# Kernel tuning notes

Hardware: AMD Instinct MI355X
Metric: run time of the kernel (lower is better)

## Reference

```python
import jax, jax.numpy as jnp
import numpy as np

N = 100000          # nodes
E = 1600000         # edges (avg degree 16)
F_IN = 128          # input node features
H1, C1 = 8, 8       # conv1: 8 heads, 8 channels/head -> 64 concat
NUM_CLASSES = 40    # conv2: 1 head, 40 channels
EPS = 1e-16         # PyG softmax denominator epsilon
NEG_SLOPE = 0.2     # PyG GATConv default leaky_relu slope


def setup_inputs() -> dict:
    key = jax.random.key(0)
    ks = jax.random.split(key, 12)
    x = jax.random.normal(ks[0], (N, F_IN), jnp.float32)
    edge_index = jax.random.randint(ks[1], (2, E), 0, N, dtype=jnp.int64)
    edge_attr = jax.random.normal(ks[2], (E, 1), jnp.float32)
    # layer 1 params (Glorot-ish scaling)
    s1 = 1.0 / np.sqrt(F_IN)
    W1 = jax.random.normal(ks[3], (F_IN, H1 * C1), jnp.float32) * s1
    a_src1 = jax.random.normal(ks[4], (H1, C1), jnp.float32) * (1.0 / np.sqrt(C1))
    a_dst1 = jax.random.normal(ks[5], (H1, C1), jnp.float32) * (1.0 / np.sqrt(C1))
    b1 = jnp.zeros((H1 * C1,), jnp.float32)
    # layer 2 params: in = 64 (conv1 concat output), 1 head, NUM_CLASSES channels
    s2 = 1.0 / np.sqrt(H1 * C1)
    W2 = jax.random.normal(ks[6], (H1 * C1, NUM_CLASSES), jnp.float32) * s2
    a_src2 = jax.random.normal(ks[7], (1, NUM_CLASSES), jnp.float32) * (1.0 / np.sqrt(NUM_CLASSES))
    a_dst2 = jax.random.normal(ks[8], (1, NUM_CLASSES), jnp.float32) * (1.0 / np.sqrt(NUM_CLASSES))
    b2 = jnp.zeros((NUM_CLASSES,), jnp.float32)
    return {"x": x, "edge_index": edge_index, "edge_attr": edge_attr,
            "W1": W1, "a_src1": a_src1, "a_dst1": a_dst1, "b1": b1,
            "W2": W2, "a_src2": a_src2, "a_dst2": a_dst2, "b2": b2}


def gat_conv(x, src, dst, W, a_s, a_d, b, heads, out_ch):
    """PyG GATConv: linear -> per-edge leaky-relu attention -> dst softmax -> scatter-add."""
    n = x.shape[0]
    h = (x @ W).reshape(n, heads, out_ch)                 # [N,H,C]
    alpha_s = jnp.sum(h * a_s, axis=-1)                   # [N,H]
    alpha_d = jnp.sum(h * a_d, axis=-1)                   # [N,H]
    e = jax.nn.leaky_relu(alpha_s[src] + alpha_d[dst], NEG_SLOPE)  # [Etot,H]
    # segment softmax over incoming edges per destination node
    m = jax.ops.segment_max(e, dst, num_segments=n)       # [N,H]
    e = jnp.exp(e - m[dst])
    denom = jax.ops.segment_sum(e, dst, num_segments=n)   # [N,H]
    alpha = e / (denom[dst] + EPS)                        # [Etot,H]
    msg = h[src] * alpha[:, :, None]                      # [Etot,H,C]
    out = jax.ops.segment_sum(msg, dst, num_segments=n)   # [N,H,C]
    return out.reshape(n, heads * out_ch) + b             # concat heads + bias


def reference(x, edge_index, edge_attr, W1, a_src1, a_dst1, b1, W2, a_src2, a_dst2, b2):
    n = x.shape[0]
    # PyG GATConv adds self-loops by default
    loops = jnp.arange(n, dtype=edge_index.dtype)
    src = jnp.concatenate([edge_index[0], loops])
    dst = jnp.concatenate([edge_index[1], loops])
    x = x.astype(jnp.float32)
    x1 = jax.nn.elu(gat_conv(x, src, dst, W1, a_src1, a_dst1, b1, H1, C1))
    x2 = jax.nn.elu(gat_conv(x1, src, dst, W2, a_src2, a_dst2, b2, 1, NUM_CLASSES))
    return x2
```

## Files before the change

### kernel.cpp

```cpp
#include <hip/hip_runtime.h>
#include <math.h>

#define NN 100000
#define NE 1600000
#define NETOT (NE + NN)
#define FIN 128
#define H1N 8
#define D1 64
#define NC 40
#define LNT 64
#define LOG2E 1.44269504088896f

#define BSH 9
#define BNODES 512
#define NBUC ((NN + BNODES - 1) / BNODES)
#define EPB 4096
#define NBLKA ((NE + EPB - 1) / EPB)
#define BCAP 9216

__device__ __forceinline__ float leakyf(float x) { return x >= 0.0f ? x : 0.2f * x; }
__device__ __forceinline__ float eluf(float x)   { return x > 0.0f ? x : expm1f(x); }
__device__ __forceinline__ float exp2fast(float x) { return __builtin_amdgcn_exp2f(x); }

__device__ __forceinline__ unsigned short f2bf(float f) {
  unsigned u = __float_as_uint(f);
  u += 0x7fffu + ((u >> 16) & 1u);
  return (unsigned short)(u >> 16);
}
__device__ __forceinline__ float bflo(unsigned u) { return __uint_as_float(u << 16); }
__device__ __forceinline__ float bfhi(unsigned u) { return __uint_as_float(u & 0xffff0000u); }

__global__ void k_detect(const long long* __restrict__ ei, int* __restrict__ flag) {
  if (blockIdx.x == 0 && threadIdx.x == 0) {
    int is64 = 1;
    for (int i = 0; i < 16; ++i) {
      long long v = ei[i];
      if (v < 0 || v >= NN) is64 = 0;
    }
    *flag = is64;
  }
}

__global__ __launch_bounds__(256) void k_passA(const void* __restrict__ ei,
                        const int* __restrict__ flag,
                        unsigned int* __restrict__ subbuf, int* __restrict__ bcnt) {
  __shared__ unsigned int   pay[EPB];
  __shared__ unsigned short bk[EPB];
  __shared__ unsigned int   spay[EPB];
  __shared__ unsigned short sbk[EPB];
  __shared__ int hist[256];
  __shared__ int lstart[256];
  __shared__ int cur[256];
  __shared__ int gbase[256];
  int t = threadIdx.x;
  int e0 = blockIdx.x * EPB;
  int cnt = min(EPB, NE - e0);
  hist[t] = 0;
  __syncthreads();
  bool f64 = (*flag) != 0;
  for (int i = t; i < cnt; i += 256) {
    int s, d;
    if (f64) {
      const long long* p = (const long long*)ei;
      s = (int)p[e0 + i]; d = (int)p[NE + e0 + i];
    } else {
      const int* p = (const int*)ei;
      s = p[e0 + i]; d = p[NE + e0 + i];
    }
    int b = d >> BSH;
    pay[i] = ((unsigned)s << BSH) | (unsigned)(d & (BNODES - 1));
    bk[i] = (unsigned short)b;
    atomicAdd(&hist[b], 1);
  }
  __syncthreads();
  int v = hist[t];
  lstart[t] = v;
  __syncthreads();
  for (int st = 1; st < 256; st <<= 1) {
    int xv = (t >= st) ? lstart[t - st] : 0;
    __syncthreads();
    lstart[t] += xv;
    __syncthreads();
  }
  int excl = lstart[t] - v;
  __syncthreads();
  lstart[t] = excl;
  cur[t] = excl;
  gbase[t] = (v > 0) ? atomicAdd(&bcnt[t], v) : 0;
  __syncthreads();
  for (int i = t; i < cnt; i += 256) {
    int b = bk[i];
    int pos = atomicAdd(&cur[b], 1);
    spay[pos] = pay[i];
    sbk[pos] = (unsigned short)b;
  }
  __syncthreads();
  for (int i = t; i < cnt; i += 256) {
    int b = sbk[i];
    int o = gbase[b] + (i - lstart[b]);
    if (o < BCAP) subbuf[(size_t)b * BCAP + o] = spay[i];
  }
}

__global__ void k_bucketsum(const int* __restrict__ bcnt, int* __restrict__ bucket_base,
                            int* __restrict__ row_start) {
  __shared__ int sh[256];
  int t = threadIdx.x;
  int tot = 0;
  if (t < NBUC) {
    int d0 = t << BSH;
    int nloc = min(BNODES, NN - d0);
    tot = nloc + min(bcnt[t], BCAP);
  }
  sh[t] = tot;
  __syncthreads();
  for (int s = 1; s < 256; s <<= 1) {
    int x = (t >= s) ? sh[t - s] : 0;
    __syncthreads();
    sh[t] += x;
    __syncthreads();
  }
  if (t < NBUC) bucket_base[t] = sh[t] - tot;
  if (t == NBUC - 1) row_start[NN] = sh[t];
}

__global__ __launch_bounds__(256) void k_passB(const int* __restrict__ bcnt,
                       const unsigned int* __restrict__ subbuf,
                       const int* __restrict__ bucket_base,
                       int* __restrict__ row_start, int* __restrict__ csr) {
  __shared__ int hist[BNODES];
  __shared__ int ps[256];
  __shared__ int cur[BNODES];
  int b = blockIdx.x, t = threadIdx.x;
  int d0 = b << BSH;
  int nloc = min(BNODES, NN - d0);
  hist[t] = 0; hist[t + 256] = 0;
  __syncthreads();
  int cnt = min(bcnt[b], BCAP);
  const unsigned int* sb = subbuf + (size_t)b * BCAP;
  for (int i = t; i < cnt; i += 256)
    atomicAdd(&hist[sb[i] & (BNODES - 1)], 1);
  __syncthreads();
  int j0 = 2 * t, j1 = 2 * t + 1;
  int s0 = (j0 < nloc) ? hist[j0] + 1 : 0;
  int s1 = (j1 < nloc) ? hist[j1] + 1 : 0;
  int pairsum = s0 + s1;
  ps[t] = pairsum;
  __syncthreads();
  for (int s = 1; s < 256; s <<= 1) {
    int x = (t >= s) ? ps[t - s] : 0;
    __syncthreads();
    ps[t] += x;
    __syncthreads();
  }
  int excl = ps[t] - pairsum + bucket_base[b];
  if (j0 < nloc) {
    row_start[d0 + j0] = excl;
    csr[excl] = d0 + j0;
    cur[j0] = excl + 1;
  }
  if (j1 < nloc) {
    int rs = excl + s0;
    row_start[d0 + j1] = rs;
    csr[rs] = d0 + j1;
    cur[j1] = rs + 1;
  }
  __syncthreads();
  for (int i = t; i < cnt; i += 256) {
    unsigned u = sb[i];
    int pos = atomicAdd(&cur[u & (BNODES - 1)], 1);
    csr[pos] = (int)(u >> BSH);
  }
}

#define XS1(node, k) xs[(node) * FIN + ((k) ^ ((node) & 31))]
__global__ void k_lin1(const float* __restrict__ x, const float* __restrict__ W,
                       const float* __restrict__ aw_s, const float* __restrict__ aw_d,
                       unsigned short* __restrict__ h, float* __restrict__ als,
                       float* __restrict__ ald) {
  __shared__ float ws[FIN * D1];
  __shared__ float xs[LNT * FIN];
  int t = threadIdx.x;
  int base = blockIdx.x * LNT;
  for (int i = t; i < FIN * D1; i += 256) ws[i] = W[i];
  for (int i = t; i < LNT * FIN; i += 256) {
    int node = i >> 7, k = i & 127;
    int gn = base + node;
    if (gn >= NN) gn = NN - 1;
    XS1(node, k) = x[(size_t)gn * FIN + k];
  }
  __syncthreads();
  int head = t & 7, ng = t >> 3;
  int n0l = ng * 2, n1l = n0l + 1;
  float acc0[8] = {0, 0, 0, 0, 0, 0, 0, 0};
  float acc1[8] = {0, 0, 0, 0, 0, 0, 0, 0};
  #pragma unroll 4
  for (int k = 0; k < FIN; ++k) {
    float x0 = XS1(n0l, k);
    float x1v = XS1(n1l, k);
    const float4* wr = (const float4*)&ws[k * D1 + head * 8];
    float4 wa = wr[0], wb = wr[1];
    acc0[0] = fmaf(x0, wa.x, acc0[0]); acc1[0] = fmaf(x1v, wa.x, acc1[0]);
    acc0[1] = fmaf(x0, wa.y, acc0[1]); acc1[1] = fmaf(x1v, wa.y, acc1[1]);
    acc0[2] = fmaf(x0, wa.z, acc0[2]); acc1[2] = fmaf(x1v, wa.z, acc1[2]);
    acc0[3] = fmaf(x0, wa.w, acc0[3]); acc1[3] = fmaf(x1v, wa.w, acc1[3]);
    acc0[4] = fmaf(x0, wb.x, acc0[4]); acc1[4] = fmaf(x1v, wb.x, acc1[4]);
    acc0[5] = fmaf(x0, wb.y, acc0[5]); acc1[5] = fmaf(x1v, wb.y, acc1[5]);
    acc0[6] = fmaf(x0, wb.z, acc0[6]); acc1[6] = fmaf(x1v, wb.z, acc1[6]);
    acc0[7] = fmaf(x0, wb.w, acc0[7]); acc1[7] = fmaf(x1v, wb.w, acc1[7]);
  }
  int n0 = base + n0l, n1 = base + n1l;
  float aws[8], awd[8];
  #pragma unroll
  for (int c = 0; c < 8; ++c) { aws[c] = aw_s[head * 8 + c]; awd[c] = aw_d[head * 8 + c]; }
  if (n0 < NN) {
    float s = 0.f, d = 0.f;
    #pragma unroll
    for (int c = 0; c < 8; ++c) {
      h[(size_t)n0 * D1 + head * 8 + c] = f2bf(acc0[c]);
      s = fmaf(acc0[c], aws[c], s);
      d = fmaf(acc0[c], awd[c], d);
    }
    als[n0 * H1N + head] = s * LOG2E;
    ald[n0 * H1N + head] = d * LOG2E;
  }
  if (n1 < NN) {
    float s = 0.f, d = 0.f;
    #pragma unroll
    for (int c = 0; c < 8; ++c) {
      h[(size_t)n1 * D1 + head * 8 + c] = f2bf(acc1[c]);
      s = fmaf(acc1[c], aws[c], s);
      d = fmaf(acc1[c], awd[c], d);
    }
    als[n1 * H1N + head] = s * LOG2E;
    ald[n1 * H1N + head] = d * LOG2E;
  }
}

#define XS2(node, k) xs[(node) * D1 + ((k) ^ ((node) & 31))]
__global__ void k_lin2(const unsigned int* __restrict__ x1bf, const float* __restrict__ W,
                       const float* __restrict__ aw_s, const float* __restrict__ aw_d,
                       unsigned short* __restrict__ h, float* __restrict__ als,
                       float* __restrict__ ald) {
  __shared__ float ws[D1 * D1];
  __shared__ float xs[LNT * D1];
  int t = threadIdx.x;
  int base = blockIdx.x * LNT;
  for (int i = t; i < D1 * D1; i += 256) {
    int k = i >> 6, c = i & 63;
    ws[i] = (c < NC) ? W[k * NC + c] : 0.f;
  }
  for (int i = t; i < LNT * 32; i += 256) {
    int node = i >> 5, kd = i & 31;
    int gn = base + node;
    if (gn >= NN) gn = NN - 1;
    unsigned u = x1bf[(size_t)gn * 32 + kd];
    XS2(node, 2 * kd)     = bflo(u);
    XS2(node, 2 * kd + 1) = bfhi(u);
  }
  __syncthreads();
  int g = t & 7, ng = t >> 3;
  int n0l = ng * 2, n1l = n0l + 1;
  float acc0[8] = {0, 0, 0, 0, 0, 0, 0, 0};
  float acc1[8] = {0, 0, 0, 0, 0, 0, 0, 0};
  #pragma unroll 4
  for (int k = 0; k < D1; ++k) {
    float x0 = XS2(n0l, k);
    float x1v = XS2(n1l, k);
    const float4* wr = (const float4*)&ws[k * D1 + g * 8];
    float4 wa = wr[0], wb = wr[1];
    acc0[0] = fmaf(x0, wa.x, acc0[0]); acc1[0] = fmaf(x1v, wa.x, acc1[0]);
    acc0[1] = fmaf(x0, wa.y, acc0[1]); acc1[1] = fmaf(x1v, wa.y, acc1[1]);
    acc0[2] = fmaf(x0, wa.z, acc0[2]); acc1[2] = fmaf(x1v, wa.z, acc1[2]);
    acc0[3] = fmaf(x0, wa.w, acc0[3]); acc1[3] = fmaf(x1v, wa.w, acc1[3]);
    acc0[4] = fmaf(x0, wb.x, acc0[4]); acc1[4] = fmaf(x1v, wb.x, acc1[4]);
    acc0[5] = fmaf(x0, wb.y, acc0[5]); acc1[5] = fmaf(x1v, wb.y, acc1[5]);
    acc0[6] = fmaf(x0, wb.z, acc0[6]); acc1[6] = fmaf(x1v, wb.z, acc1[6]);
    acc0[7] = fmaf(x0, wb.w, acc0[7]); acc1[7] = fmaf(x1v, wb.w, acc1[7]);
  }
  int n0 = base + n0l, n1 = base + n1l;
  float aws[8], awd[8];
  #pragma unroll
  for (int c = 0; c < 8; ++c) {
    int col = g * 8 + c;
    aws[c] = (col < NC) ? aw_s[col] : 0.f;
    awd[c] = (col < NC) ? aw_d[col] : 0.f;
  }
  float s0 = 0.f, d0 = 0.f, s1 = 0.f, d1 = 0.f;
  #pragma unroll
  for (int c = 0; c < 8; ++c) {
    s0 = fmaf(acc0[c], aws[c], s0); d0 = fmaf(acc0[c], awd[c], d0);
    s1 = fmaf(acc1[c], aws[c], s1); d1 = fmaf(acc1[c], awd[c], d1);
  }
  s0 += __shfl_xor(s0, 1); d0 += __shfl_xor(d0, 1); s1 += __shfl_xor(s1, 1); d1 += __shfl_xor(d1, 1);
  s0 += __shfl_xor(s0, 2); d0 += __shfl_xor(d0, 2); s1 += __shfl_xor(s1, 2); d1 += __shfl_xor(d1, 2);
  s0 += __shfl_xor(s0, 4); d0 += __shfl_xor(d0, 4); s1 += __shfl_xor(s1, 4); d1 += __shfl_xor(d1, 4);
  if (n0 < NN && g < 5) {
    #pragma unroll
    for (int c = 0; c < 8; ++c) h[(size_t)n0 * NC + g * 8 + c] = f2bf(acc0[c]);
  }
  if (n1 < NN && g < 5) {
    #pragma unroll
    for (int c = 0; c < 8; ++c) h[(size_t)n1 * NC + g * 8 + c] = f2bf(acc1[c]);
  }
  if (g == 0) {
    if (n0 < NN) { als[n0] = s0 * LOG2E; ald[n0] = d0 * LOG2E; }
    if (n1 < NN) { als[n1] = s1 * LOG2E; ald[n1] = d1 * LOG2E; }
  }
}

__global__ void k_node1(const int* __restrict__ row_start, const int* __restrict__ csr,
                        const unsigned short* __restrict__ h, const float* __restrict__ als,
                        const float* __restrict__ ald, const float* __restrict__ b,
                        unsigned int* __restrict__ x1bf) {
  __shared__ float pl[4][2][32 * 9];
  int wid = threadIdx.x >> 6, half = (threadIdx.x >> 5) & 1, c2 = threadIdx.x & 31;
  int n = blockIdx.x * 8 + wid * 2 + half;
  float* pw = pl[wid][half];
  const unsigned int* h32 = (const unsigned int*)h;
  int r0 = row_start[n], r1 = row_start[n + 1];
  int hd = c2 >> 2;
  const float4* adp = (const float4*)(ald + (size_t)n * H1N);
  float4 ad0 = adp[0], ad1 = adp[1];
  float S = 0.f;
  float alo0 = 0.f, ahi0 = 0.f, alo1 = 0.f, ahi1 = 0.f;
  float alo2 = 0.f, ahi2 = 0.f, alo3 = 0.f, ahi3 = 0.f;
  for (int kb = r0; kb < r1; kb += 32) {
    int cnt = min(32, r1 - kb);
    if (c2 < cnt) {
      int sk = csr[kb + c2];
      const float4* ap = (const float4*)(als + (size_t)sk * H1N);
      float4 a0 = ap[0], a1 = ap[1];
      pw[c2 * 9 + 0] = exp2fast(leakyf(a0.x + ad0.x));
      pw[c2 * 9 + 1] = exp2fast(leakyf(a0.y + ad0.y));
      pw[c2 * 9 + 2] = exp2fast(leakyf(a0.z + ad0.z));
      pw[c2 * 9 + 3] = exp2fast(leakyf(a0.w + ad0.w));
      pw[c2 * 9 + 4] = exp2fast(leakyf(a1.x + ad1.x));
      pw[c2 * 9 + 5] = exp2fast(leakyf(a1.y + ad1.y));
      pw[c2 * 9 + 6] = exp2fast(leakyf(a1.z + ad1.z));
      pw[c2 * 9 + 7] = exp2fast(leakyf(a1.w + ad1.w));
      pw[c2 * 9 + 8] = __int_as_float(sk);
    }
    asm volatile("s_waitcnt lgkmcnt(0)" ::: "memory");
    int j = 0;
    for (; j + 4 <= cnt; j += 4) {
      int s0 = __float_as_int(pw[(j + 0) * 9 + 8]);
      int s1 = __float_as_int(pw[(j + 1) * 9 + 8]);
      int s2 = __float_as_int(pw[(j + 2) * 9 + 8]);
      int s3 = __float_as_int(pw[(j + 3) * 9 + 8]);
      float p0 = pw[(j + 0) * 9 + hd], p1 = pw[(j + 1) * 9 + hd];
      float p2 = pw[(j + 2) * 9 + hd], p3 = pw[(j + 3) * 9 + hd];
      unsigned u0 = h32[(unsigned)s0 * 32 + c2];
      unsigned u1 = h32[(unsigned)s1 * 32 + c2];
      unsigned u2 = h32[(unsigned)s2 * 32 + c2];
      unsigned u3 = h32[(unsigned)s3 * 32 + c2];
      alo0 = fmaf(p0, bflo(u0), alo0); ahi0 = fmaf(p0, bfhi(u0), ahi0);
      alo1 = fmaf(p1, bflo(u1), alo1); ahi1 = fmaf(p1, bfhi(u1), ahi1);
      alo2 = fmaf(p2, bflo(u2), alo2); ahi2 = fmaf(p2, bfhi(u2), ahi2);
      alo3 = fmaf(p3, bflo(u3), alo3); ahi3 = fmaf(p3, bfhi(u3), ahi3);
      S += (p0 + p1) + (p2 + p3);
    }
    for (; j < cnt; ++j) {
      int s0 = __float_as_int(pw[j * 9 + 8]);
      float p0 = pw[j * 9 + hd];
      unsigned u0 = h32[(unsigned)s0 * 32 + c2];
      alo0 = fmaf(p0, bflo(u0), alo0); ahi0 = fmaf(p0, bfhi(u0), ahi0);
      S += p0;
    }
  }
  float alo = (alo0 + alo1) + (alo2 + alo3);
  float ahi = (ahi0 + ahi1) + (ahi2 + ahi3);
  float inv = 1.0f / (S + 1e-16f);
  float ox = eluf(alo * inv + b[2 * c2 + 0]);
  float oy = eluf(ahi * inv + b[2 * c2 + 1]);
  x1bf[(size_t)n * 32 + c2] = (unsigned)f2bf(ox) | ((unsigned)f2bf(oy) << 16);
}

__global__ void k_node2(const int* __restrict__ row_start, const int* __restrict__ csr,
                        const unsigned short* __restrict__ h, const float* __restrict__ als,
                        const float* __restrict__ ald, const float* __restrict__ b,
                        float* __restrict__ out) {
  __shared__ float pl[4][2][32 * 3];
  int wid = threadIdx.x >> 6, half = (threadIdx.x >> 5) & 1, c2 = threadIdx.x & 31;
  int n = blockIdx.x * 8 + wid * 2 + half;
  float* pw = pl[wid][half];
  const unsigned int* h32 = (const unsigned int*)h;
  int r0 = row_start[n], r1 = row_start[n + 1];
  int cl = c2 < 20 ? c2 : 19;
  float aldn = ald[n];
  float S = 0.f;
  float alo0 = 0.f, ahi0 = 0.f, alo1 = 0.f, ahi1 = 0.f;
  float alo2 = 0.f, ahi2 = 0.f, alo3 = 0.f, ahi3 = 0.f;
  for (int kb = r0; kb < r1; kb += 32) {
    int cnt = min(32, r1 - kb);
    if (c2 < cnt) {
      int sk = csr[kb + c2];
      pw[c2 * 3 + 0] = exp2fast(leakyf(als[sk] + aldn));
      pw[c2 * 3 + 1] = __int_as_float(sk);
    }
    asm volatile("s_waitcnt lgkmcnt(0)" ::: "memory");
    int j = 0;
    for (; j + 4 <= cnt; j += 4) {
      int s0 = __float_as_int(pw[(j + 0) * 3 + 1]);
      int s1 = __float_as_int(pw[(j + 1) * 3 + 1]);
      int s2 = __float_as_int(pw[(j + 2) * 3 + 1]);
      int s3 = __float_as_int(pw[(j + 3) * 3 + 1]);
      float p0 = pw[(j + 0) * 3], p1 = pw[(j + 1) * 3];
      float p2 = pw[(j + 2) * 3], p3 = pw[(j + 3) * 3];
      unsigned u0 = h32[(unsigned)s0 * 20 + cl];
      unsigned u1 = h32[(unsigned)s1 * 20 + cl];
      unsigned u2 = h32[(unsigned)s2 * 20 + cl];
      unsigned u3 = h32[(unsigned)s3 * 20 + cl];
      alo0 = fmaf(p0, bflo(u0), alo0); ahi0 = fmaf(p0, bfhi(u0), ahi0);
      alo1 = fmaf(p1, bflo(u1), alo1); ahi1 = fmaf(p1, bfhi(u1), ahi1);
      alo2 = fmaf(p2, bflo(u2), alo2); ahi2 = fmaf(p2, bfhi(u2), ahi2);
      alo3 = fmaf(p3, bflo(u3), alo3); ahi3 = fmaf(p3, bfhi(u3), ahi3);
      S += (p0 + p1) + (p2 + p3);
    }
    for (; j < cnt; ++j) {
      int s0 = __float_as_int(pw[j * 3 + 1]);
      float p0 = pw[j * 3];
      unsigned u0 = h32[(unsigned)s0 * 20 + cl];
      alo0 = fmaf(p0, bflo(u0), alo0); ahi0 = fmaf(p0, bfhi(u0), ahi0);
      S += p0;
    }
  }
  float alo = (alo0 + alo1) + (alo2 + alo3);
  float ahi = (ahi0 + ahi1) + (ahi2 + ahi3);
  if (c2 < 20) {
    float inv = 1.0f / (S + 1e-16f);
    float2 o;
    o.x = eluf(alo * inv + b[2 * c2 + 0]);
    o.y = eluf(ahi * inv + b[2 * c2 + 1]);
    ((float2*)out)[(size_t)n * 20 + c2] = o;
  }
}

extern "C" void kernel_launch(void* const* d_in, const int* in_sizes, int n_in,
                              void* d_out, int out_size, void* d_ws, size_t ws_size,
                              hipStream_t stream) {
  const float* x    = (const float*)d_in[0];
  const void*  ei   = d_in[1];
  const float* W1   = (const float*)d_in[3];
  const float* as1w = (const float*)d_in[4];
  const float* ad1w = (const float*)d_in[5];
  const float* b1   = (const float*)d_in[6];
  const float* W2   = (const float*)d_in[7];
  const float* as2w = (const float*)d_in[8];
  const float* ad2w = (const float*)d_in[9];
  const float* b2   = (const float*)d_in[10];
  float* out = (float*)d_out;

  char* w = (char*)d_ws;
  size_t off = 0;
  auto carve = [&](size_t bytes) -> void* {
    void* r = w + off;
    off += (bytes + 255) & ~(size_t)255;
    return r;
  };
  int*            flag        = (int*)carve(256);
  int*            bcnt        = (int*)carve((size_t)NBUC * 4);
  int*            bucket_base = (int*)carve((size_t)NBUC * 4);
  unsigned int*   subbuf      = (unsigned int*)carve((size_t)NBUC * BCAP * 4);
  int*            row_start   = (int*)carve((size_t)(NN + 1) * 4);
  int*            csr         = (int*)carve((size_t)NETOT * 4);
  unsigned short* h1          = (unsigned short*)carve((size_t)NN * D1 * 2);
  float*          als1        = (float*)carve((size_t)NN * H1N * 4);
  float*          ald1        = (float*)carve((size_t)NN * H1N * 4);
  unsigned int*   x1bf        = (unsigned int*)carve((size_t)NN * 32 * 4);
  unsigned short* h2 = h1; float* als2 = als1; float* ald2 = ald1;

  const int LB = (NN + LNT - 1) / LNT;

  k_detect<<<1, 64, 0, stream>>>((const long long*)ei, flag);
  (void)hipMemsetAsync(bcnt, 0, (size_t)NBUC * 4, stream);
  k_passA<<<NBLKA, 256, 0, stream>>>(ei, flag, subbuf, bcnt);
  k_bucketsum<<<1, 256, 0, stream>>>(bcnt, bucket_base, row_start);
  k_passB<<<NBUC, 256, 0, stream>>>(bcnt, subbuf, bucket_base, row_start, csr);

  k_lin1<<<LB, 256, 0, stream>>>(x, W1, as1w, ad1w, h1, als1, ald1);
  k_node1<<<NN / 8, 256, 0, stream>>>(row_start, csr, h1, als1, ald1, b1, x1bf);

  k_lin2<<<LB, 256, 0, stream>>>(x1bf, W2, as2w, ad2w, h2, als2, ald2);
  k_node2<<<NN / 8, 256, 0, stream>>>(row_start, csr, h2, als2, ald2, b2, out);
}
```

Measured before the change: 217.8 us.

## Fuse edge bucketing pass with layer-1 linear into one heterogeneous launch

```diff
diff --git a/kernel.cpp b/kernel.cpp
--- a/kernel.cpp
+++ b/kernel.cpp
@@ -17,6 +17,7 @@
 #define EPB 4096
 #define NBLKA ((NE + EPB - 1) / EPB)
 #define BCAP 9216
+#define LB1 ((NN + LNT - 1) / LNT)
 
 __device__ __forceinline__ float leakyf(float x) { return x >= 0.0f ? x : 0.2f * x; }
 __device__ __forceinline__ float eluf(float x)   { return x > 0.0f ? x : expm1f(x); }
@@ -41,64 +42,115 @@
   }
 }
 
-__global__ __launch_bounds__(256) void k_passA(const void* __restrict__ ei,
-                        const int* __restrict__ flag,
-                        unsigned int* __restrict__ subbuf, int* __restrict__ bcnt) {
-  __shared__ unsigned int   pay[EPB];
-  __shared__ unsigned short bk[EPB];
-  __shared__ unsigned int   spay[EPB];
-  __shared__ unsigned short sbk[EPB];
-  __shared__ int hist[256];
-  __shared__ int lstart[256];
-  __shared__ int cur[256];
-  __shared__ int gbase[256];
+#define XS1(node, k) xs[(node) * FIN + ((k) ^ ((node) & 31))]
+__global__ __launch_bounds__(512) void k_fusedA(
+    const void* __restrict__ ei, const int* __restrict__ flag,
+    unsigned int* __restrict__ subbuf, int* __restrict__ bcnt,
+    const float* __restrict__ x, const float* __restrict__ W,
+    const float* __restrict__ aw_s, const float* __restrict__ aw_d,
+    unsigned short* __restrict__ h, float* __restrict__ als,
+    float* __restrict__ ald) {
+  __shared__ __align__(16) char smem[65536];
   int t = threadIdx.x;
-  int e0 = blockIdx.x * EPB;
-  int cnt = min(EPB, NE - e0);
-  hist[t] = 0;
-  __syncthreads();
-  bool f64 = (*flag) != 0;
-  for (int i = t; i < cnt; i += 256) {
-    int s, d;
-    if (f64) {
-      const long long* p = (const long long*)ei;
-      s = (int)p[e0 + i]; d = (int)p[NE + e0 + i];
-    } else {
-      const int* p = (const int*)ei;
-      s = p[e0 + i]; d = p[NE + e0 + i];
-    }
-    int b = d >> BSH;
-    pay[i] = ((unsigned)s << BSH) | (unsigned)(d & (BNODES - 1));
-    bk[i] = (unsigned short)b;
-    atomicAdd(&hist[b], 1);
-  }
-  __syncthreads();
-  int v = hist[t];
-  lstart[t] = v;
-  __syncthreads();
-  for (int st = 1; st < 256; st <<= 1) {
-    int xv = (t >= st) ? lstart[t - st] : 0;
-    __syncthreads();
-    lstart[t] += xv;
-    __syncthreads();
-  }
-  int excl = lstart[t] - v;
-  __syncthreads();
-  lstart[t] = excl;
-  cur[t] = excl;
-  gbase[t] = (v > 0) ? atomicAdd(&bcnt[t], v) : 0;
-  __syncthreads();
-  for (int i = t; i < cnt; i += 256) {
-    int b = bk[i];
-    int pos = atomicAdd(&cur[b], 1);
-    spay[pos] = pay[i];
-    sbk[pos] = (unsigned short)b;
-  }
-  __syncthreads();
-  for (int i = t; i < cnt; i += 256) {
-    int b = sbk[i];
-    int o = gbase[b] + (i - lstart[b]);
-    if (o < BCAP) subbuf[(size_t)b * BCAP + o] = spay[i];
+  if (blockIdx.x < NBLKA) {
+    unsigned int*   pay    = (unsigned int*)smem;
+    unsigned int*   spay   = pay + EPB;
+    unsigned short* bk     = (unsigned short*)(spay + EPB);
+    unsigned short* sbk    = bk + EPB;
+    int*            hist   = (int*)(sbk + EPB);
+    int*            lstart = hist + 256;
+    int*            cur    = lstart + 256;
+    int*            gbase  = cur + 256;
+    int e0 = blockIdx.x * EPB;
+    int cnt = min(EPB, NE - e0);
+    if (t < 256) hist[t] = 0;
+    __syncthreads();
+    bool f64 = (*flag) != 0;
+    for (int i = t; i < cnt; i += 512) {
+      int s, d;
+      if (f64) {
+        const long long* p = (const long long*)ei;
+        s = (int)p[e0 + i]; d = (int)p[NE + e0 + i];
+      } else {
+        const int* p = (const int*)ei;
+        s = p[e0 + i]; d = p[NE + e0 + i];
+      }
+      int b = d >> BSH;
+      pay[i] = ((unsigned)s << BSH) | (unsigned)(d & (BNODES - 1));
+      bk[i] = (unsigned short)b;
+      atomicAdd(&hist[b], 1);
+    }
+    __syncthreads();
+    int v = 0;
+    if (t < 256) { v = hist[t]; lstart[t] = v; }
+    __syncthreads();
+    for (int st = 1; st < 256; st <<= 1) {
+      int xv = (t < 256 && t >= st) ? lstart[t - st] : 0;
+      __syncthreads();
+      if (t < 256) lstart[t] += xv;
+      __syncthreads();
+    }
+    int excl = 0;
+    if (t < 256) excl = lstart[t] - v;
+    __syncthreads();
+    if (t < 256) {
+      lstart[t] = excl;
+      cur[t] = excl;
+      gbase[t] = (v > 0) ? atomicAdd(&bcnt[t], v) : 0;
+    }
+    __syncthreads();
+    for (int i = t; i < cnt; i += 512) {
+      int b = bk[i];
+      int pos = atomicAdd(&cur[b], 1);
+      spay[pos] = pay[i];
+      sbk[pos] = (unsigned short)b;
+    }
+    __syncthreads();
+    for (int i = t; i < cnt; i += 512) {
+      int b = sbk[i];
+      int o = gbase[b] + (i - lstart[b]);
+      if (o < BCAP) subbuf[(size_t)b * BCAP + o] = spay[i];
+    }
+  } else {
+    float* ws = (float*)smem;
+    float* xs = ws + FIN * D1;
+    int base = (blockIdx.x - NBLKA) * LNT;
+    for (int i = t; i < FIN * D1; i += 512) ws[i] = W[i];
+    for (int i = t; i < LNT * FIN; i += 512) {
+      int node = i >> 7, k = i & 127;
+      int gn = base + node;
+      if (gn >= NN) gn = NN - 1;
+      XS1(node, k) = x[(size_t)gn * FIN + k];
+    }
+    __syncthreads();
+    int head = t & 7, nl = t >> 3;
+    float acc[8] = {0, 0, 0, 0, 0, 0, 0, 0};
+    #pragma unroll 4
+    for (int k = 0; k < FIN; ++k) {
+      float x0 = XS1(nl, k);
+      const float4* wr = (const float4*)&ws[k * D1 + head * 8];
+      float4 wa = wr[0], wb = wr[1];
+      acc[0] = fmaf(x0, wa.x, acc[0]);
+      acc[1] = fmaf(x0, wa.y, acc[1]);
+      acc[2] = fmaf(x0, wa.z, acc[2]);
+      acc[3] = fmaf(x0, wa.w, acc[3]);
+      acc[4] = fmaf(x0, wb.x, acc[4]);
+      acc[5] = fmaf(x0, wb.y, acc[5]);
+      acc[6] = fmaf(x0, wb.z, acc[6]);
+      acc[7] = fmaf(x0, wb.w, acc[7]);
+    }
+    int n0 = base + nl;
+    if (n0 < NN) {
+      float s = 0.f, d = 0.f;
+      #pragma unroll
+      for (int c = 0; c < 8; ++c) {
+        h[(size_t)n0 * D1 + head * 8 + c] = f2bf(acc[c]);
+        s = fmaf(acc[c], aw_s[head * 8 + c], s);
+        d = fmaf(acc[c], aw_d[head * 8 + c], d);
+      }
+      als[n0 * H1N + head] = s * LOG2E;
+      ald[n0 * H1N + head] = d * LOG2E;
+    }
   }
 }
 
@@ -173,84 +225,21 @@
   }
 }
 
-#define XS1(node, k) xs[(node) * FIN + ((k) ^ ((node) & 31))]
-__global__ void k_lin1(const float* __restrict__ x, const float* __restrict__ W,
-                       const float* __restrict__ aw_s, const float* __restrict__ aw_d,
-                       unsigned short* __restrict__ h, float* __restrict__ als,
-                       float* __restrict__ ald) {
-  __shared__ float ws[FIN * D1];
-  __shared__ float xs[LNT * FIN];
-  int t = threadIdx.x;
-  int base = blockIdx.x * LNT;
-  for (int i = t; i < FIN * D1; i += 256) ws[i] = W[i];
-  for (int i = t; i < LNT * FIN; i += 256) {
-    int node = i >> 7, k = i & 127;
-    int gn = base + node;
-    if (gn >= NN) gn = NN - 1;
-    XS1(node, k) = x[(size_t)gn * FIN + k];
-  }
-  __syncthreads();
-  int head = t & 7, ng = t >> 3;
-  int n0l = ng * 2, n1l = n0l + 1;
-  float acc0[8] = {0, 0, 0, 0, 0, 0, 0, 0};
-  float acc1[8] = {0, 0, 0, 0, 0, 0, 0, 0};
-  #pragma unroll 4
-  for (int k = 0; k < FIN; ++k) {
-    float x0 = XS1(n0l, k);
-    float x1v = XS1(n1l, k);
-    const float4* wr = (const float4*)&ws[k * D1 + head * 8];
-    float4 wa = wr[0], wb = wr[1];
-    acc0[0] = fmaf(x0, wa.x, acc0[0]); acc1[0] = fmaf(x1v, wa.x, acc1[0]);
-    acc0[1] = fmaf(x0, wa.y, acc0[1]); acc1[1] = fmaf(x1v, wa.y, acc1[1]);
-    acc0[2] = fmaf(x0, wa.z, acc0[2]); acc1[2] = fmaf(x1v, wa.z, acc1[2]);
-    acc0[3] = fmaf(x0, wa.w, acc0[3]); acc1[3] = fmaf(x1v, wa.w, acc1[3]);
-    acc0[4] = fmaf(x0, wb.x, acc0[4]); acc1[4] = fmaf(x1v, wb.x, acc1[4]);
-    acc0[5] = fmaf(x0, wb.y, acc0[5]); acc1[5] = fmaf(x1v, wb.y, acc1[5]);
-    acc0[6] = fmaf(x0, wb.z, acc0[6]); acc1[6] = fmaf(x1v, wb.z, acc1[6]);
-    acc0[7] = fmaf(x0, wb.w, acc0[7]); acc1[7] = fmaf(x1v, wb.w, acc1[7]);
-  }
-  int n0 = base + n0l, n1 = base + n1l;
-  float aws[8], awd[8];
-  #pragma unroll
-  for (int c = 0; c < 8; ++c) { aws[c] = aw_s[head * 8 + c]; awd[c] = aw_d[head * 8 + c]; }
-  if (n0 < NN) {
-    float s = 0.f, d = 0.f;
-    #pragma unroll
-    for (int c = 0; c < 8; ++c) {
-      h[(size_t)n0 * D1 + head * 8 + c] = f2bf(acc0[c]);
-      s = fmaf(acc0[c], aws[c], s);
-      d = fmaf(acc0[c], awd[c], d);
-    }
-    als[n0 * H1N + head] = s * LOG2E;
-    ald[n0 * H1N + head] = d * LOG2E;
-  }
-  if (n1 < NN) {
-    float s = 0.f, d = 0.f;
-    #pragma unroll
-    for (int c = 0; c < 8; ++c) {
-      h[(size_t)n1 * D1 + head * 8 + c] = f2bf(acc1[c]);
-      s = fmaf(acc1[c], aws[c], s);
-      d = fmaf(acc1[c], awd[c], d);
-    }
-    als[n1 * H1N + head] = s * LOG2E;
-    ald[n1 * H1N + head] = d * LOG2E;
-  }
-}
-
 #define XS2(node, k) xs[(node) * D1 + ((k) ^ ((node) & 31))]
-__global__ void k_lin2(const unsigned int* __restrict__ x1bf, const float* __restrict__ W,
-                       const float* __restrict__ aw_s, const float* __restrict__ aw_d,
-                       unsigned short* __restrict__ h, float* __restrict__ als,
-                       float* __restrict__ ald) {
+__global__ __launch_bounds__(512) void k_lin2(
+    const unsigned int* __restrict__ x1bf, const float* __restrict__ W,
+    const float* __restrict__ aw_s, const float* __restrict__ aw_d,
+    unsigned short* __restrict__ h, float* __restrict__ als,
+    float* __restrict__ ald) {
   __shared__ float ws[D1 * D1];
   __shared__ float xs[LNT * D1];
   int t = threadIdx.x;
   int base = blockIdx.x * LNT;
-  for (int i = t; i < D1 * D1; i += 256) {
+  for (int i = t; i < D1 * D1; i += 512) {
     int k = i >> 6, c = i & 63;
     ws[i] = (c < NC) ? W[k * NC + c] : 0.f;
   }
-  for (int i = t; i < LNT * 32; i += 256) {
+  for (int i = t; i < LNT * 32; i += 512) {
     int node = i >> 5, kd = i & 31;
     int gn = base + node;
     if (gn >= NN) gn = NN - 1;
@@ -259,53 +248,41 @@
     XS2(node, 2 * kd + 1) = bfhi(u);
   }
   __syncthreads();
-  int g = t & 7, ng = t >> 3;
-  int n0l = ng * 2, n1l = n0l + 1;
-  float acc0[8] = {0, 0, 0, 0, 0, 0, 0, 0};
-  float acc1[8] = {0, 0, 0, 0, 0, 0, 0, 0};
+  int g = t & 7, nl = t >> 3;
+  float acc[8] = {0, 0, 0, 0, 0, 0, 0, 0};
   #pragma unroll 4
   for (int k = 0; k < D1; ++k) {
-    float x0 = XS2(n0l, k);
-    float x1v = XS2(n1l, k);
+    float x0 = XS2(nl, k);
     const float4* wr = (const float4*)&ws[k * D1 + g * 8];
     float4 wa = wr[0], wb = wr[1];
-    acc0[0] = fmaf(x0, wa.x, acc0[0]); acc1[0] = fmaf(x1v, wa.x, acc1[0]);
-    acc0[1] = fmaf(x0, wa.y, acc0[1]); acc1[1] = fmaf(x1v, wa.y, acc1[1]);
-    acc0[2] = fmaf(x0, wa.z, acc0[2]); acc1[2] = fmaf(x1v, wa.z, acc1[2]);
-    acc0[3] = fmaf(x0, wa.w, acc0[3]); acc1[3] = fmaf(x1v, wa.w, acc1[3]);
-    acc0[4] = fmaf(x0, wb.x, acc0[4]); acc1[4] = fmaf(x1v, wb.x, acc1[4]);
-    acc0[5] = fmaf(x0, wb.y, acc0[5]); acc1[5] = fmaf(x1v, wb.y, acc1[5]);
-    acc0[6] = fmaf(x0, wb.z, acc0[6]); acc1[6] = fmaf(x1v, wb.z, acc1[6]);
-    acc0[7] = fmaf(x0, wb.w, acc0[7]); acc1[7] = fmaf(x1v, wb.w, acc1[7]);
-  }
-  int n0 = base + n0l, n1 = base + n1l;
-  float aws[8], awd[8];
+    acc[0] = fmaf(x0, wa.x, acc[0]);
+    acc[1] = fmaf(x0, wa.y, acc[1]);
+    acc[2] = fmaf(x0, wa.z, acc[2]);
+    acc[3] = fmaf(x0, wa.w, acc[3]);
+    acc[4] = fmaf(x0, wb.x, acc[4]);
+    acc[5] = fmaf(x0, wb.y, acc[5]);
+    acc[6] = fmaf(x0, wb.z, acc[6]);
+    acc[7] = fmaf(x0, wb.w, acc[7]);
+  }
+  int n0 = base + nl;
+  float s = 0.f, d = 0.f;
   #pragma unroll
   for (int c = 0; c < 8; ++c) {
     int col = g * 8 + c;
-    aws[c] = (col < NC) ? aw_s[col] : 0.f;
-    awd[c] = (col < NC) ? aw_d[col] : 0.f;
-  }
-  float s0 = 0.f, d0 = 0.f, s1 = 0.f, d1 = 0.f;
-  #pragma unroll
-  for (int c = 0; c < 8; ++c) {
-    s0 = fmaf(acc0[c], aws[c], s0); d0 = fmaf(acc0[c], awd[c], d0);
-    s1 = fmaf(acc1[c], aws[c], s1); d1 = fmaf(acc1[c], awd[c], d1);
-  }
-  s0 += __shfl_xor(s0, 1); d0 += __shfl_xor(d0, 1); s1 += __shfl_xor(s1, 1); d1 += __shfl_xor(d1, 1);
-  s0 += __shfl_xor(s0, 2); d0 += __shfl_xor(d0, 2); s1 += __shfl_xor(s1, 2); d1 += __shfl_xor(d1, 2);
-  s0 += __shfl_xor(s0, 4); d0 += __shfl_xor(d0, 4); s1 += __shfl_xor(s1, 4); d1 += __shfl_xor(d1, 4);
-  if (n0 < NN && g < 5) {
-    #pragma unroll
-    for (int c = 0; c < 8; ++c) h[(size_t)n0 * NC + g * 8 + c] = f2bf(acc0[c]);
-  }
-  if (n1 < NN && g < 5) {
-    #pragma unroll
-    for (int c = 0; c < 8; ++c) h[(size_t)n1 * NC + g * 8 + c] = f2bf(acc1[c]);
-  }
-  if (g == 0) {
-    if (n0 < NN) { als[n0] = s0 * LOG2E; ald[n0] = d0 * LOG2E; }
-    if (n1 < NN) { als[n1] = s1 * LOG2E; ald[n1] = d1 * LOG2E; }
+    float aws = (col < NC) ? aw_s[col] : 0.f;
+    float awd = (col < NC) ? aw_d[col] : 0.f;
+    s = fmaf(acc[c], aws, s);
+    d = fmaf(acc[c], awd, d);
+  }
+  s += __shfl_xor(s, 1); d += __shfl_xor(d, 1);
+  s += __shfl_xor(s, 2); d += __shfl_xor(d, 2);
+  s += __shfl_xor(s, 4); d += __shfl_xor(d, 4);
+  if (n0 < NN) {
+    if (g < 5) {
+      #pragma unroll
+      for (int c = 0; c < 8; ++c) h[(size_t)n0 * NC + g * 8 + c] = f2bf(acc[c]);
+    }
+    if (g == 0) { als[n0] = s * LOG2E; ald[n0] = d * LOG2E; }
   }
 }
 
@@ -470,17 +447,17 @@
   unsigned int*   x1bf        = (unsigned int*)carve((size_t)NN * 32 * 4);
   unsigned short* h2 = h1; float* als2 = als1; float* ald2 = ald1;
 
-  const int LB = (NN + LNT - 1) / LNT;
-
   k_detect<<<1, 64, 0, stream>>>((const long long*)ei, flag);
   (void)hipMemsetAsync(bcnt, 0, (size_t)NBUC * 4, stream);
-  k_passA<<<NBLKA, 256, 0, stream>>>(ei, flag, subbuf, bcnt);
+
+  k_fusedA<<<NBLKA + LB1, 512, 0, stream>>>(ei, flag, subbuf, bcnt,
+                                            x, W1, as1w, ad1w, h1, als1, ald1);
+
   k_bucketsum<<<1, 256, 0, stream>>>(bcnt, bucket_base, row_start);
   k_passB<<<NBUC, 256, 0, stream>>>(bcnt, subbuf, bucket_base, row_start, csr);
 
-  k_lin1<<<LB, 256, 0, stream>>>(x, W1, as1w, ad1w, h1, als1, ald1);
   k_node1<<<NN / 8, 256, 0, stream>>>(row_start, csr, h1, als1, ald1, b1, x1bf);
 
-  k_lin2<<<LB, 256, 0, stream>>>(x1bf, W2, as2w, ad2w, h2, als2, ald2);
+  k_lin2<<<LB1, 512, 0, stream>>>(x1bf, W2, as2w, ad2w, h2, als2, ald2);
   k_node2<<<NN / 8, 256, 0, stream>>>(row_start, csr, h2, als2, ald2, b2, out);
 }
```

New measurement: 206.2 us. 5.3% less time.
